# Performance work log

Hardware: AMD Instinct MI355X
Metric: run time of the kernel (lower is better)

The kernel has to match this reference:

```python
import jax, jax.numpy as jnp
import numpy as np

B, S, E, H = 16, 256, 4096, 16
D = E // H  # 256; module's matmul pattern requires S == D and B == H


def setup_inputs() -> dict:
    rng = jax.random.key(0)
    k0, k1, k2, k3, k4 = jax.random.split(rng, 5)
    return {
        "query": jax.random.normal(k0, (B, S, E), jnp.float32),
        "key": jax.random.normal(k1, (B, S, E), jnp.float32),
        "value": jax.random.normal(k2, (B, S, E), jnp.float32),
        # out_proj: torch nn.Linear(E, E) -> y = x @ W.T + b
        "out_w": jax.random.normal(k3, (E, E), jnp.float32) * 0.02,
        "out_b": jnp.zeros((E,), jnp.float32),
    }


def reference(query, key, value, out_w, out_b):
    scale = D ** -0.5
    # split heads: [B, S, E] -> [B, H, S, D]
    q = (query * scale).reshape(B, S, H, D).transpose(0, 2, 1, 3)
    k = key.reshape(B, S, H, D).transpose(0, 2, 1, 3)
    v = value.reshape(B, S, H, D).transpose(0, 2, 1, 3)
    # torch.matmul(q_head, k_head) with NO transpose: contracts q's D with k's S
    # (valid because S == D). aw: [B, H, S, D]
    aw = jnp.einsum('bhit,bhtj->bhij', q, k)
    # attn_weights.transpose(0, 1): [B, H, ...] -> [H, B, ...]
    aw = jnp.swapaxes(aw, 0, 1)
    # eval mode path: softmax over last dim (no dropout)
    aw = jax.nn.softmax(aw, axis=-1)
    # torch.matmul(aw [H,B,S,D], v [B,H,S,D]): batch dims broadcast because B == H,
    # pairing elementwise -> out[x,y] = aw[x,y] @ v[x,y]
    out = jnp.einsum('xyit,xytj->xyij', aw, v)
    # transpose(1, 2) then reshape to (B, S, E)
    out = jnp.swapaxes(out, 1, 2).reshape(B, S, E)
    # out_proj
    return out @ out_w.T + out_b
```

## Files before the change

kernel.cpp:

```cpp
#include <hip/hip_runtime.h>

#define AS1 __attribute__((address_space(1)))
#define AS3 __attribute__((address_space(3)))

typedef __bf16 bf16x8 __attribute__((ext_vector_type(8)));
typedef float f32x4 __attribute__((ext_vector_type(4)));

__device__ __forceinline__ unsigned short f2bf(float f) {
  unsigned int u = __builtin_bit_cast(unsigned int, f);
  u += 0x7fffu + ((u >> 16) & 1u);
  return (unsigned short)(u >> 16);
}

__global__ __launch_bounds__(256) void kv_transpose(
    const float* __restrict__ key, const float* __restrict__ value,
    unsigned short* __restrict__ KT2, unsigned short* __restrict__ VT2) {
  __shared__ float tr[32 * 33];
  const int tid = threadIdx.x;
  const int ts  = blockIdx.y;
  const int pp  = blockIdx.x >> 3;
  const int s   = blockIdx.x & 7;
  const int b   = ts ? (pp >> 4) : (pp & 15);
  const int h   = ts ? (pp & 15) : (pp >> 4);
  const float* src = (ts ? value : key) + ((size_t)(b * 256 + s * 32)) * 4096 + h * 256;
  unsigned short* dst = (ts ? VT2 : KT2) + (size_t)(pp * 8 + s) * 8192;
  const int tt = tid >> 3;
  const int q8 = tid & 7;
  for (int jb = 0; jb < 8; ++jb) {
    float4 v = *(const float4*)(src + (size_t)tt * 4096 + jb * 32 + q8 * 4);
    tr[tt * 33 + q8 * 4 + 0] = v.x;
    tr[tt * 33 + q8 * 4 + 1] = v.y;
    tr[tt * 33 + q8 * 4 + 2] = v.z;
    tr[tt * 33 + q8 * 4 + 3] = v.w;
    __syncthreads();
    ushort4 o;
    o.x = f2bf(tr[(q8 * 4 + 0) * 33 + tt]);
    o.y = f2bf(tr[(q8 * 4 + 1) * 33 + tt]);
    o.z = f2bf(tr[(q8 * 4 + 2) * 33 + tt]);
    o.w = f2bf(tr[(q8 * 4 + 3) * 33 + tt]);
    *(ushort4*)(dst + (jb * 32 + tt) * 32 + q8 * 4) = o;
    __syncthreads();
  }
}

__global__ __launch_bounds__(256, 2) void attn_kernel(
    const float* __restrict__ qin, const unsigned short* __restrict__ KT2,
    const unsigned short* __restrict__ VT2, unsigned short* __restrict__ attn) {
  __shared__ __align__(16) unsigned short kv[8192];
  __shared__ __align__(16) unsigned short plds[4 * 16 * 264];

  const int tid  = threadIdx.x;
  const int lane = tid & 63;
  const int wave = tid >> 6;
  const int li   = lane & 15;
  const int ks   = lane >> 4;

  const int bid = blockIdx.x;
  const int pp  = (bid & 7) * 32 + ((bid >> 3) & 31);
  const int ib  = bid >> 8;
  const int x = pp >> 4, y = pp & 15;
  const int i0 = ib * 64 + wave * 16;

  bf16x8 qf[8];
  {
    const float* qrow = qin + ((size_t)(y * 256 + i0 + li)) * 4096 + x * 256 + ks * 8;
#pragma unroll
    for (int s = 0; s < 8; ++s) {
      float4 v0 = *(const float4*)(qrow + s * 32);
      float4 v1 = *(const float4*)(qrow + s * 32 + 4);
      union { bf16x8 v; unsigned short u[8]; } t;
      t.u[0] = f2bf(v0.x * 0.0625f); t.u[1] = f2bf(v0.y * 0.0625f);
      t.u[2] = f2bf(v0.z * 0.0625f); t.u[3] = f2bf(v0.w * 0.0625f);
      t.u[4] = f2bf(v1.x * 0.0625f); t.u[5] = f2bf(v1.y * 0.0625f);
      t.u[6] = f2bf(v1.z * 0.0625f); t.u[7] = f2bf(v1.w * 0.0625f);
      qf[s] = t.v;
    }
  }

  const f32x4 vzero = {0.f, 0.f, 0.f, 0.f};
  f32x4 sacc[16];
#pragma unroll
  for (int f = 0; f < 16; ++f) sacc[f] = vzero;

  const unsigned short* ktile = KT2 + (size_t)pp * 65536;
#pragma unroll
  for (int s = 0; s < 8; ++s) {
    __syncthreads();
#pragma unroll
    for (int cc = 0; cc < 4; ++cc) {
      const unsigned short* g = ktile + (size_t)s * 8192 + (cc * 256 + tid) * 8;
      __builtin_amdgcn_global_load_lds((AS1 unsigned int*)g,
          (AS3 unsigned int*)((AS3 char*)kv + cc * 4096 + wave * 1024), 16, 0, 0);
    }
    __syncthreads();
#pragma unroll
    for (int f = 0; f < 16; ++f) {
      bf16x8 bfr = *(const bf16x8*)&kv[(f * 16 + li) * 32 + ks * 8];
      sacc[f] = __builtin_amdgcn_mfma_f32_16x16x32_bf16(qf[s], bfr, sacc[f], 0, 0, 0);
    }
  }

  float sm[4];
#pragma unroll
  for (int qi = 0; qi < 4; ++qi) {
    float m = sacc[0][qi];
#pragma unroll
    for (int f = 1; f < 16; ++f) m = fmaxf(m, sacc[f][qi]);
    m = fmaxf(m, __shfl_xor(m, 1));
    m = fmaxf(m, __shfl_xor(m, 2));
    m = fmaxf(m, __shfl_xor(m, 4));
    m = fmaxf(m, __shfl_xor(m, 8));
    float ssum = 0.f;
#pragma unroll
    for (int f = 0; f < 16; ++f) {
      float pv = __expf(sacc[f][qi] - m);
      sacc[f][qi] = pv;
      ssum += pv;
    }
    ssum += __shfl_xor(ssum, 1);
    ssum += __shfl_xor(ssum, 2);
    ssum += __shfl_xor(ssum, 4);
    ssum += __shfl_xor(ssum, 8);
    sm[qi] = ssum;
  }

  unsigned short* pw = plds + wave * 4224;
#pragma unroll
  for (int f = 0; f < 16; ++f)
#pragma unroll
    for (int qi = 0; qi < 4; ++qi)
      pw[(ks * 4 + qi) * 264 + f * 16 + li] = f2bf(sacc[f][qi]);

  f32x4 oacc[16];
#pragma unroll
  for (int f = 0; f < 16; ++f) oacc[f] = vzero;
  const unsigned short* vtile = VT2 + (size_t)pp * 65536;
  const unsigned short* pr = plds + wave * 4224 + li * 264;
#pragma unroll
  for (int s2 = 0; s2 < 8; ++s2) {
    __syncthreads();
#pragma unroll
    for (int cc = 0; cc < 4; ++cc) {
      const unsigned short* g = vtile + (size_t)s2 * 8192 + (cc * 256 + tid) * 8;
      __builtin_amdgcn_global_load_lds((AS1 unsigned int*)g,
          (AS3 unsigned int*)((AS3 char*)kv + cc * 4096 + wave * 1024), 16, 0, 0);
    }
    __syncthreads();
    bf16x8 afr = *(const bf16x8*)&pr[s2 * 32 + ks * 8];
#pragma unroll
    for (int f = 0; f < 16; ++f) {
      bf16x8 bfr = *(const bf16x8*)&kv[(f * 16 + li) * 32 + ks * 8];
      oacc[f] = __builtin_amdgcn_mfma_f32_16x16x32_bf16(afr, bfr, oacc[f], 0, 0, 0);
    }
  }

  float rs4[4];
#pragma unroll
  for (int qi = 0; qi < 4; ++qi) rs4[qi] = 1.0f / sm[qi];
  unsigned short* abase = attn + (size_t)(x * 256 + i0 + ks * 4) * 4096 + y * 256 + li;
#pragma unroll
  for (int f = 0; f < 16; ++f)
#pragma unroll
    for (int qi = 0; qi < 4; ++qi)
      abase[(size_t)qi * 4096 + f * 16] = f2bf(oacc[f][qi] * rs4[qi]);
}

__global__ __launch_bounds__(256) void convw(const float* __restrict__ w,
                                             unsigned short* __restrict__ o) {
  const int i = blockIdx.x * 256 + threadIdx.x;
  const float4* s = (const float4*)w + (size_t)i * 2;
  float4 v0 = s[0], v1 = s[1];
  uint4 pk;
  pk.x = (unsigned)f2bf(v0.x) | ((unsigned)f2bf(v0.y) << 16);
  pk.y = (unsigned)f2bf(v0.z) | ((unsigned)f2bf(v0.w) << 16);
  pk.z = (unsigned)f2bf(v1.x) | ((unsigned)f2bf(v1.y) << 16);
  pk.w = (unsigned)f2bf(v1.z) | ((unsigned)f2bf(v1.w) << 16);
  *((uint4*)o + i) = pk;
}

__global__ __launch_bounds__(512, 2) void proj_gemm8(
    const unsigned short* __restrict__ A, const unsigned short* __restrict__ W,
    const float* __restrict__ bias, float* __restrict__ out) {
  __shared__ __align__(1024) char lds[131072];

  const int tid  = threadIdx.x;
  const int lane = tid & 63;
  const int w    = tid >> 6;
  const int li   = lane & 15;
  const int ks   = lane >> 4;
  const int wr   = w >> 2;
  const int wc   = w & 3;
  const int LB   = li * 64 + ((ks * 16) ^ ((((li >> 1) & 3)) << 4));

  const int bid = blockIdx.x;
  const int swz = (bid & 7) * 32 + (bid >> 3);
  const int m0b = (swz >> 4) * 256, n0b = (swz & 15) * 256;

  unsigned srcA[2], srcB[2];
  int dstP[2];
#pragma unroll
  for (int j = 0; j < 2; ++j) {
    int P = tid * 16 + j * 8192;
    int L = P ^ ((P >> 3) & 0x30);
    int row = L >> 6, col = L & 63;
    srcA[j] = (unsigned)((m0b + row) * 8192 + col);
    srcB[j] = (unsigned)((n0b + row) * 8192 + col);
    dstP[j] = P;
  }
  const char* Ac = (const char*)A;
  const char* Wc = (const char*)W;
  AS3 char* L3 = (AS3 char*)lds;

  const f32x4 vzero = {0.f, 0.f, 0.f, 0.f};
  f32x4 acc[8][4];
#pragma unroll
  for (int m = 0; m < 8; ++m)
#pragma unroll
    for (int n = 0; n < 4; ++n) acc[m][n] = vzero;

#define STAGE(T) do {                                                          \
    const int _sl = ((T) & 3) * 32768; const unsigned _ko = (unsigned)(T) * 64u; \
    _Pragma("unroll") for (int j = 0; j < 2; ++j) {                            \
      __builtin_amdgcn_global_load_lds((AS1 unsigned int*)(Ac + srcA[j] + _ko),\
          (AS3 unsigned int*)(L3 + _sl + dstP[j]), 16, 0, 0);                  \
      __builtin_amdgcn_global_load_lds((AS1 unsigned int*)(Wc + srcB[j] + _ko),\
          (AS3 unsigned int*)(L3 + _sl + 16384 + dstP[j]), 16, 0, 0);          \
    } } while (0)
#define RD_A(S, M) (*(const bf16x8*)(lds + (S) + wr * 8192 + (M) * 1024 + LB))
#define RD_B(S, N) (*(const bf16x8*)(lds + (S) + 16384 + wc * 4096 + (N) * 1024 + LB))
#define MFMA(a, b, c) __builtin_amdgcn_mfma_f32_16x16x32_bf16((a), (b), (c), 0, 0, 0)

  bf16x8 A0[4], A1[4], Bc[4], Bn[4];

  STAGE(0); STAGE(1); STAGE(2);
  asm volatile("s_waitcnt vmcnt(4)" ::: "memory");
  __builtin_amdgcn_s_barrier();
#pragma unroll
  for (int m = 0; m < 4; ++m) A0[m] = RD_A(0, m);
#pragma unroll
  for (int n = 0; n < 4; ++n) Bc[n] = RD_B(0, n);

#define TILE(T, BU, BN2) do {                                                  \
    const int cs = ((T) & 3) * 32768;                                          \
    const int ns = (((T) + 1) & 3) * 32768;                                    \
    const int ss = ((T) + 3 < 128) ? (T) + 3 : 127;                            \
    _Pragma("unroll") for (int m = 0; m < 4; ++m) A1[m] = RD_A(cs, m + 4);     \
    _Pragma("unroll") for (int n = 0; n < 4; ++n) BN2[n] = RD_B(ns, n);        \
    STAGE(ss);                                                                 \
    __builtin_amdgcn_s_barrier();                                              \
    asm volatile("s_waitcnt lgkmcnt(8)" ::: "memory");                         \
    __builtin_amdgcn_s_setprio(1);                                             \
    _Pragma("unroll") for (int m = 0; m < 4; ++m)                              \
      _Pragma("unroll") for (int n = 0; n < 4; ++n)                            \
        acc[m][n] = MFMA(A0[m], BU[n], acc[m][n]);                             \
    __builtin_amdgcn_s_setprio(0);                                             \
    asm volatile("s_waitcnt vmcnt(8)" ::: "memory");                           \
    __builtin_amdgcn_s_barrier();                                              \
    _Pragma("unroll") for (int m = 0; m < 4; ++m) A0[m] = RD_A(ns, m);         \
    __builtin_amdgcn_s_barrier();                                              \
    asm volatile("s_waitcnt lgkmcnt(8)" ::: "memory");                         \
    __builtin_amdgcn_s_setprio(1);                                             \
    _Pragma("unroll") for (int m = 0; m < 4; ++m)                              \
      _Pragma("unroll") for (int n = 0; n < 4; ++n)                            \
        acc[m + 4][n] = MFMA(A1[m], BU[n], acc[m + 4][n]);                     \
    __builtin_amdgcn_s_setprio(0);                                             \
    asm volatile("s_waitcnt vmcnt(4)" ::: "memory");                           \
    __builtin_amdgcn_s_barrier();                                              \
  } while (0)

  for (int it = 0; it < 64; ++it) {
    TILE(2 * it,     Bc, Bn);
    TILE(2 * it + 1, Bn, Bc);
  }

  float bv[4];
#pragma unroll
  for (int n = 0; n < 4; ++n) bv[n] = bias[n0b + wc * 64 + n * 16 + li];
#pragma unroll
  for (int m = 0; m < 8; ++m) {
#pragma unroll
    for (int qi = 0; qi < 4; ++qi) {
      const int row = m0b + wr * 128 + m * 16 + ks * 4 + qi;
      float* orow = out + (size_t)row * 4096 + n0b + wc * 64 + li;
#pragma unroll
      for (int n = 0; n < 4; ++n) orow[n * 16] = acc[m][n][qi] + bv[n];
    }
  }
#undef STAGE
#undef RD_A
#undef RD_B
#undef MFMA
#undef TILE
}

extern "C" void kernel_launch(void* const* d_in, const int* in_sizes, int n_in,
                              void* d_out, int out_size, void* d_ws, size_t ws_size,
                              hipStream_t stream) {
  const float* q = (const float*)d_in[0];
  const float* k = (const float*)d_in[1];
  const float* v = (const float*)d_in[2];
  const float* w = (const float*)d_in[3];
  const float* b = (const float*)d_in[4];
  float* out = (float*)d_out;
  char* ws = (char*)d_ws;

  unsigned short* attn = (unsigned short*)ws;
  unsigned short* KT2  = (unsigned short*)(ws + (size_t)33554432);
  unsigned short* VT2  = (unsigned short*)(ws + (size_t)67108864);
  unsigned short* wbf  = KT2;

  kv_transpose<<<dim3(2048, 2), 256, 0, stream>>>(k, v, KT2, VT2);
  attn_kernel<<<1024, 256, 0, stream>>>(q, KT2, VT2, attn);
  convw<<<8192, 256, 0, stream>>>(w, wbf);
  proj_gemm8<<<256, 512, 0, stream>>>(attn, wbf, b, out);
}
```

Baseline: 238.8 us.

## Simplify projection GEMM main loop and change LDS swizzle pattern

Replaces the hand-interleaved two-phase tile loop, which used register double-buffering of A/B fragments and several barriers per tile, with a single loop that reads all fragments for a tile, issues the next prefetch, then runs all 32 MFMAs behind one barrier. The LDS XOR swizzle for both the global-to-LDS writes and the fragment reads is changed to a simpler pattern. This cuts barrier count and code complexity, but gives up overlap of LDS reads with MFMA work. The new swizzle may also raise LDS bank conflicts.

New measurement: 236.2 us. No clear change (-1.1%).

```diff
diff --git a/kernel.cpp b/kernel.cpp
--- a/kernel.cpp
+++ b/kernel.cpp
@@ -190,22 +190,22 @@
   const int ks   = lane >> 4;
   const int wr   = w >> 2;
   const int wc   = w & 3;
-  const int LB   = li * 64 + ((ks * 16) ^ ((((li >> 1) & 3)) << 4));
+  const int LB   = (li * 64 + ks * 16) ^ (((li >> 3) & 1) << 5);
 
   const int bid = blockIdx.x;
   const int swz = (bid & 7) * 32 + (bid >> 3);
   const int m0b = (swz >> 4) * 256, n0b = (swz & 15) * 256;
 
-  unsigned srcA[2], srcB[2];
+  unsigned sA[2], sB[2];
   int dstP[2];
 #pragma unroll
   for (int j = 0; j < 2; ++j) {
-    int P = tid * 16 + j * 8192;
-    int L = P ^ ((P >> 3) & 0x30);
+    int P = j * 8192 + tid * 16;
+    int L = P ^ (((P >> 9) & 1) << 5);
     int row = L >> 6, col = L & 63;
-    srcA[j] = (unsigned)((m0b + row) * 8192 + col);
-    srcB[j] = (unsigned)((n0b + row) * 8192 + col);
     dstP[j] = P;
+    sA[j] = (unsigned)((m0b + row) * 8192 + col);
+    sB[j] = (unsigned)((n0b + row) * 8192 + col);
   }
   const char* Ac = (const char*)A;
   const char* Wc = (const char*)W;
@@ -218,59 +218,45 @@
 #pragma unroll
     for (int n = 0; n < 4; ++n) acc[m][n] = vzero;
 
-#define STAGE(T) do {                                                          \
-    const int _sl = ((T) & 3) * 32768; const unsigned _ko = (unsigned)(T) * 64u; \
+#define STAGE(kt, slot) do {                                                   \
+    const unsigned _ko = (unsigned)(kt) * 64u;                                 \
+    const int _sl = (slot) * 32768;                                            \
     _Pragma("unroll") for (int j = 0; j < 2; ++j) {                            \
-      __builtin_amdgcn_global_load_lds((AS1 unsigned int*)(Ac + srcA[j] + _ko),\
+      __builtin_amdgcn_global_load_lds((AS1 unsigned int*)(Ac + sA[j] + _ko),  \
           (AS3 unsigned int*)(L3 + _sl + dstP[j]), 16, 0, 0);                  \
-      __builtin_amdgcn_global_load_lds((AS1 unsigned int*)(Wc + srcB[j] + _ko),\
+      __builtin_amdgcn_global_load_lds((AS1 unsigned int*)(Wc + sB[j] + _ko),  \
           (AS3 unsigned int*)(L3 + _sl + 16384 + dstP[j]), 16, 0, 0);          \
     } } while (0)
 #define RD_A(S, M) (*(const bf16x8*)(lds + (S) + wr * 8192 + (M) * 1024 + LB))
 #define RD_B(S, N) (*(const bf16x8*)(lds + (S) + 16384 + wc * 4096 + (N) * 1024 + LB))
 #define MFMA(a, b, c) __builtin_amdgcn_mfma_f32_16x16x32_bf16((a), (b), (c), 0, 0, 0)
 
-  bf16x8 A0[4], A1[4], Bc[4], Bn[4];
-
-  STAGE(0); STAGE(1); STAGE(2);
-  asm volatile("s_waitcnt vmcnt(4)" ::: "memory");
+  STAGE(0, 0); STAGE(1, 1); STAGE(2, 2);
+  asm volatile("s_waitcnt vmcnt(8)" ::: "memory");
   __builtin_amdgcn_s_barrier();
-#pragma unroll
-  for (int m = 0; m < 4; ++m) A0[m] = RD_A(0, m);
-#pragma unroll
-  for (int n = 0; n < 4; ++n) Bc[n] = RD_B(0, n);
-
-#define TILE(T, BU, BN2) do {                                                  \
-    const int cs = ((T) & 3) * 32768;                                          \
-    const int ns = (((T) + 1) & 3) * 32768;                                    \
-    const int ss = ((T) + 3 < 128) ? (T) + 3 : 127;                            \
-    _Pragma("unroll") for (int m = 0; m < 4; ++m) A1[m] = RD_A(cs, m + 4);     \
-    _Pragma("unroll") for (int n = 0; n < 4; ++n) BN2[n] = RD_B(ns, n);        \
-    STAGE(ss);                                                                 \
-    __builtin_amdgcn_s_barrier();                                              \
-    asm volatile("s_waitcnt lgkmcnt(8)" ::: "memory");                         \
-    __builtin_amdgcn_s_setprio(1);                                             \
-    _Pragma("unroll") for (int m = 0; m < 4; ++m)                              \
-      _Pragma("unroll") for (int n = 0; n < 4; ++n)                            \
-        acc[m][n] = MFMA(A0[m], BU[n], acc[m][n]);                             \
-    __builtin_amdgcn_s_setprio(0);                                             \
-    asm volatile("s_waitcnt vmcnt(8)" ::: "memory");                           \
-    __builtin_amdgcn_s_barrier();                                              \
-    _Pragma("unroll") for (int m = 0; m < 4; ++m) A0[m] = RD_A(ns, m);         \
-    __builtin_amdgcn_s_barrier();                                              \
-    asm volatile("s_waitcnt lgkmcnt(8)" ::: "memory");                         \
-    __builtin_amdgcn_s_setprio(1);                                             \
-    _Pragma("unroll") for (int m = 0; m < 4; ++m)                              \
-      _Pragma("unroll") for (int n = 0; n < 4; ++n)                            \
-        acc[m + 4][n] = MFMA(A1[m], BU[n], acc[m + 4][n]);                     \
-    __builtin_amdgcn_s_setprio(0);                                             \
-    asm volatile("s_waitcnt vmcnt(4)" ::: "memory");                           \
-    __builtin_amdgcn_s_barrier();                                              \
-  } while (0)
-
-  for (int it = 0; it < 64; ++it) {
-    TILE(2 * it,     Bc, Bn);
-    TILE(2 * it + 1, Bn, Bc);
+
+  for (int t = 0; t < 128; ++t) {
+    const int sl = (t & 3) * 32768;
+    bf16x8 af[8], bf[4];
+#pragma unroll
+    for (int m = 0; m < 8; ++m) af[m] = RD_A(sl, m);
+#pragma unroll
+    for (int n = 0; n < 4; ++n) bf[n] = RD_B(sl, n);
+
+    const int kt = (t + 3 < 128) ? t + 3 : 127;
+    STAGE(kt, (t + 3) & 3);
+
+    asm volatile("s_waitcnt lgkmcnt(0)" ::: "memory");
+    __builtin_amdgcn_s_setprio(1);
+#pragma unroll
+    for (int m = 0; m < 8; ++m)
+#pragma unroll
+      for (int n = 0; n < 4; ++n)
+        acc[m][n] = MFMA(af[m], bf[n], acc[m][n]);
+    __builtin_amdgcn_s_setprio(0);
+
+    asm volatile("s_waitcnt vmcnt(8)" ::: "memory");
+    __builtin_amdgcn_s_barrier();
   }
 
   float bv[4];
@@ -290,7 +276,6 @@
 #undef RD_A
 #undef RD_B
 #undef MFMA
-#undef TILE
 }
 
 extern "C" void kernel_launch(void* const* d_in, const int* in_sizes, int n_in,
```
